# Optimization experiments

Measured on AMD Instinct MI355X. Metric: run time of the kernel, lower is better.

## Reference

```python
import jax, jax.numpy as jnp
import numpy as np

EPS = 1e-5
NEG = -1e20


def layer_norm(x, gamma, beta):
    mu = jnp.mean(x, axis=-1, keepdims=True)
    var = jnp.mean(jnp.square(x - mu), axis=-1, keepdims=True)
    return (x - mu) * jax.lax.rsqrt(var + EPS) * gamma + beta


def setup_inputs() -> dict:
    key = jax.random.key(0)
    ks = jax.random.split(key, 12)
    B, S, D, H, HD = 2, 2048, 1024, 16, 64
    hid = H * HD
    inp = {
        "q": jax.random.normal(ks[0], (B, S, D), jnp.float32),
        "k": jax.random.normal(ks[1], (B, S, D), jnp.float32),
        "v": jax.random.normal(ks[2], (B, S, D), jnp.float32),
        "mask": jax.random.randint(ks[3], (B, 1, S, S), 0, 2, jnp.int32),
        "Wq": jax.random.normal(ks[4], (D, hid), jnp.float32) * (D ** -0.5),
        "bq": jnp.zeros((hid,), jnp.float32),
        "Wk": jax.random.normal(ks[5], (D, hid), jnp.float32) * (D ** -0.5),
        "bk": jnp.zeros((hid,), jnp.float32),
        "Wv": jax.random.normal(ks[6], (D, hid), jnp.float32) * (D ** -0.5),
        "bv": jnp.zeros((hid,), jnp.float32),
        "Wo": jax.random.normal(ks[7], (hid, D), jnp.float32) * (hid ** -0.5),
        "bo": jnp.zeros((D,), jnp.float32),
        "gamma": jnp.ones((D,), jnp.float32),
        "beta": jnp.zeros((D,), jnp.float32),
    }
    return inp


def reference(q, k, v, mask, Wq, bq, Wk, bk, Wv, bv, Wo, bo, gamma, beta):
    B, S, D = q.shape
    H, HD = 16, 64
    scale = HD ** -0.5
    qh = (layer_norm(q, gamma, beta) @ Wq + bq).reshape(B, S, H, HD).transpose(0, 2, 1, 3)
    kh = (layer_norm(k, gamma, beta) @ Wk + bk).reshape(B, S, H, HD).transpose(0, 2, 1, 3)
    vh = (layer_norm(v, gamma, beta) @ Wv + bv).reshape(B, S, H, HD).transpose(0, 2, 1, 3)
    dots = jnp.einsum('bhqd,bhkd->bhqk', qh, kh)  # [B,H,S,S]
    dots = jnp.where(mask == 0, NEG, dots) * scale  # mask BEFORE scale (as in source)
    attn = jax.nn.softmax(dots, axis=-1)
    out = jnp.einsum('bhqk,bhkd->bhqd', attn, vh)  # [B,H,S,HD]
    # Faithful to `out.view(B, S, -1)` on a [B,H,S,HD]-contiguous tensor: raw reshape,
    # no head transpose.
    out = out.reshape(B, S, H * HD)
    return out @ Wo + bo
```

## Files before the change

### kernel.cpp

```cpp
#include <hip/hip_runtime.h>

typedef short short8 __attribute__((ext_vector_type(8)));
typedef float f32x4 __attribute__((ext_vector_type(4)));

#define QSCALE 0.18033688011112042f

__device__ __forceinline__ unsigned short f2bf(float f) {
  unsigned u = __builtin_bit_cast(unsigned, f);
  u += 0x7fffu + ((u >> 16) & 1u);
  return (unsigned short)(u >> 16);
}

__device__ __forceinline__ void gload16(const void* g, void* l) {
  typedef __attribute__((address_space(1))) unsigned int gas;
  typedef __attribute__((address_space(3))) unsigned int las;
  __builtin_amdgcn_global_load_lds((gas*)(unsigned long long)g,
                                   (las*)(unsigned)(unsigned long long)l, 16, 0, 0);
}

#define MFMA16(a, b, c) __builtin_amdgcn_mfma_f32_16x16x32_bf16(a, b, c, 0, 0, 0)

__global__ __launch_bounds__(256) void wtrans_kernel(
    const float* __restrict__ Wq, const float* __restrict__ Wk,
    const float* __restrict__ Wv, const float* __restrict__ Wo,
    unsigned short* __restrict__ Wt) {
  const int wsel = blockIdx.z;
  const float* W = wsel == 0 ? Wq : wsel == 1 ? Wk : wsel == 2 ? Wv : Wo;
  const float wscale = (wsel == 0) ? QSCALE : 1.0f;
  unsigned short* out = Wt + (long)wsel * 1048576;
  __shared__ float lds[64][65];
  const int t = threadIdx.x;
  const int k0 = blockIdx.x * 64, n0 = blockIdx.y * 64;
#pragma unroll
  for (int i = 0; i < 4; ++i) {
    int r = (t >> 4) + i * 16, c4 = (t & 15) * 4;
    float4 vv = *(const float4*)(W + (long)(k0 + r) * 1024 + n0 + c4);
    lds[r][c4] = vv.x; lds[r][c4 + 1] = vv.y; lds[r][c4 + 2] = vv.z; lds[r][c4 + 3] = vv.w;
  }
  __syncthreads();
#pragma unroll
  for (int i = 0; i < 16; ++i) {
    int flat = t + i * 256;
    int n = flat >> 6, kk = flat & 63;
    out[(long)(n0 + n) * 1024 + k0 + kk] = f2bf(lds[kk][n] * wscale);
  }
}

__global__ __launch_bounds__(256) void maskpack_kernel(const int* __restrict__ mask,
                                                       unsigned* __restrict__ bits) {
  const long n = 8388608;
  const long stride = (long)gridDim.x * 256;
  const int lane = threadIdx.x & 63;
  for (long i = (long)blockIdx.x * 256 + threadIdx.x; i < n; i += stride) {
    unsigned long long bal = __ballot(mask[i] != 0);
    if ((lane & 31) == 0) bits[i >> 5] = (unsigned)(bal >> (lane & 32));
  }
}

__global__ __launch_bounds__(256) void ln_kernel(
    const float* __restrict__ q, const float* __restrict__ k, const float* __restrict__ v,
    const float* __restrict__ gamma, const float* __restrict__ beta,
    unsigned short* __restrict__ lnq, unsigned short* __restrict__ lnk,
    unsigned short* __restrict__ lnv) {
  const int row = blockIdx.x, which = blockIdx.y;
  const float* x = (which == 0 ? q : which == 1 ? k : v) + (long)row * 1024;
  unsigned short* y = (which == 0 ? lnq : which == 1 ? lnk : lnv) + (long)row * 1024;
  const int t = threadIdx.x, lane = t & 63, wv = t >> 6;
  float4 xv = ((const float4*)x)[t];
  float s = xv.x + xv.y + xv.z + xv.w;
  float s2 = xv.x * xv.x + xv.y * xv.y + xv.z * xv.z + xv.w * xv.w;
#pragma unroll
  for (int off = 32; off > 0; off >>= 1) {
    s += __shfl_down(s, off);
    s2 += __shfl_down(s2, off);
  }
  __shared__ float red[8];
  if (lane == 0) { red[wv] = s; red[wv + 4] = s2; }
  __syncthreads();
  float tot = red[0] + red[1] + red[2] + red[3];
  float tot2 = red[4] + red[5] + red[6] + red[7];
  float mu = tot * (1.0f / 1024.0f);
  float var = tot2 * (1.0f / 1024.0f) - mu * mu;
  float rs = rsqrtf(var + 1e-5f);
  float4 g = ((const float4*)gamma)[t];
  float4 be = ((const float4*)beta)[t];
  ushort4 o;
  o.x = f2bf((xv.x - mu) * rs * g.x + be.x);
  o.y = f2bf((xv.y - mu) * rs * g.y + be.y);
  o.z = f2bf((xv.z - mu) * rs * g.z + be.z);
  o.w = f2bf((xv.w - mu) * rs * g.w + be.w);
  ((ushort4*)y)[t] = o;
}

template <int BM, int MODE>
__global__ __launch_bounds__(256) void gemm_kernel(
    const unsigned short* __restrict__ A0, const unsigned short* __restrict__ A1,
    const unsigned short* __restrict__ A2, const unsigned short* __restrict__ Wt,
    const float* __restrict__ b0, const float* __restrict__ b1,
    const float* __restrict__ b2, unsigned short* __restrict__ outB,
    unsigned short* __restrict__ outV, float* __restrict__ outF) {
  constexpr int BK = 64;
  constexpr int MI = BM / 32;
  const int z = blockIdx.z;
  const unsigned short* A = z == 0 ? A0 : z == 1 ? A1 : A2;
  const unsigned short* Bt = Wt + (long)z * 1048576;
  const float* bias = z == 0 ? b0 : z == 1 ? b1 : b2;
  unsigned short* outz = outB + (long)z * 4194304;
  const float bscale = (MODE == 0 && z == 0) ? QSCALE : 1.0f;

  __shared__ char lds[BM * 128 + 16384];
  char* As = lds;
  char* Bs = lds + BM * 128;
  const int tid = threadIdx.x, lane = tid & 63, w = tid >> 6;
  const int wr = w >> 1, wc = w & 1;
  const int m0 = blockIdx.x * BM, n0 = blockIdx.y * 128;
  constexpr int K = 1024;
  constexpr int ACH = BM * 8 / 256;

  f32x4 acc[MI][4] = {};
  for (int kt = 0; kt < K / BK; ++kt) {
    __syncthreads();
#pragma unroll
    for (int i = 0; i < ACH; ++i) {
      int c = tid + i * 256;
      int row = c >> 3, pg = (c & 7) ^ (row & 7);
      gload16(A + (long)(m0 + row) * K + kt * BK + pg * 8, As + c * 16);
    }
#pragma unroll
    for (int i = 0; i < 4; ++i) {
      int c = tid + i * 256;
      int row = c >> 3, pg = (c & 7) ^ (row & 7);
      gload16(Bt + (long)(n0 + row) * K + kt * BK + pg * 8, Bs + c * 16);
    }
    asm volatile("s_waitcnt vmcnt(0)" ::: "memory");
    __syncthreads();
#pragma unroll
    for (int ks = 0; ks < 2; ++ks) {
      short8 af[MI], bf[4];
#pragma unroll
      for (int mi = 0; mi < MI; ++mi) {
        int row = wr * (BM / 2) + mi * 16 + (lane & 15);
        int part = (ks * 4 + (lane >> 4)) ^ (row & 7);
        af[mi] = *(const short8*)(As + row * 128 + part * 16);
      }
#pragma unroll
      for (int ni = 0; ni < 4; ++ni) {
        int row = wc * 64 + ni * 16 + (lane & 15);
        int part = (ks * 4 + (lane >> 4)) ^ (row & 7);
        bf[ni] = *(const short8*)(Bs + row * 128 + part * 16);
      }
#pragma unroll
      for (int mi = 0; mi < MI; ++mi)
#pragma unroll
        for (int ni = 0; ni < 4; ++ni)
          acc[mi][ni] = MFMA16(af[mi], bf[ni], acc[mi][ni]);
    }
  }
#pragma unroll
  for (int mi = 0; mi < MI; ++mi) {
    int mbase = m0 + wr * (BM / 2) + mi * 16 + ((lane >> 4) << 2);
#pragma unroll
    for (int ni = 0; ni < 4; ++ni) {
      int j = n0 + wc * 64 + ni * 16 + (lane & 15);
      float bj = bias[j] * bscale;
      float t0 = acc[mi][ni][0] + bj;
      float t1 = acc[mi][ni][1] + bj;
      float t2 = acc[mi][ni][2] + bj;
      float t3 = acc[mi][ni][3] + bj;
      if constexpr (MODE == 0) {
        int b = mbase >> 11, s = mbase & 2047;
        int h = j >> 6, d = j & 63;
        if (z == 2) {
          unsigned lo, hi;
          asm("v_cvt_pk_bf16_f32 %0, %1, %2" : "=v"(lo) : "v"(t0), "v"(t1));
          asm("v_cvt_pk_bf16_f32 %0, %1, %2" : "=v"(hi) : "v"(t2), "v"(t3));
          uint2 o; o.x = lo; o.y = hi;
          *(uint2*)(outV + ((long)(b * 16 + h) * 64 + d) * 2048 + s) = o;
        } else {
          long base = (((long)(b * 16 + h)) * 2048 + s) * 64 + d;
          outz[base] = f2bf(t0);
          outz[base + 64] = f2bf(t1);
          outz[base + 128] = f2bf(t2);
          outz[base + 192] = f2bf(t3);
        }
      } else {
        outF[(long)mbase * 1024 + j] = t0;
        outF[(long)(mbase + 1) * 1024 + j] = t1;
        outF[(long)(mbase + 2) * 1024 + j] = t2;
        outF[(long)(mbase + 3) * 1024 + j] = t3;
      }
    }
  }
}

__global__ __launch_bounds__(256, 4) void attn_kernel(
    const unsigned short* __restrict__ qh, const unsigned short* __restrict__ kh,
    const unsigned short* __restrict__ vt, const unsigned* __restrict__ mbits,
    unsigned short* __restrict__ O) {
  constexpr int S = 2048, NT = 32;
  __shared__ char lds[40960];
  char* Ks = lds;
  char* Vts = lds + 16384;
  const int tid = threadIdx.x, lane = tid & 63, w = tid >> 6;
  const int g = lane >> 4, c = lane & 15;
  char* Pw = lds + 32768 + w * 2048;

  const int flat = blockIdx.y * 32 + blockIdx.x;
  const int fl2 = (flat & 7) * 128 + (flat >> 3);
  const int qb = fl2 & 31, bh = fl2 >> 5, b = bh >> 4;

  const unsigned short* qp = qh + (long)bh * S * 64;
  const unsigned short* kp = kh + (long)bh * S * 64;
  const unsigned short* vp = vt + (long)bh * 64 * S;
  unsigned short* op = O + (long)bh * S * 64;
  const unsigned* mrow = mbits + (long)b * S * 64;
  const int q0 = qb * 64 + w * 16;
  const int myq = q0 + c;

  short8 bq_[2];
#pragma unroll
  for (int ds = 0; ds < 2; ++ds)
    bq_[ds] = *(const short8*)(qp + (long)myq * 64 + ds * 32 + g * 8);

  f32x4 o_acc[4] = {};
  float lpart = 0.f;

#define STAGE(KT, BUF)                                                              \
  {                                                                                 \
    _Pragma("unroll") for (int i = 0; i < 2; ++i) {                                 \
      int cc = tid + i * 256;                                                       \
      int row = cc >> 3, pg = (cc & 7) ^ (row & 7);                                 \
      gload16(kp + (long)((KT)*64 + row) * 64 + pg * 8, Ks + (BUF)*8192 + cc * 16); \
    }                                                                               \
    _Pragma("unroll") for (int i = 0; i < 2; ++i) {                                 \
      int cc = tid + i * 256;                                                       \
      int row = cc >> 3, pg = (cc & 7) ^ (row & 7);                                 \
      gload16(vp + (long)row * S + (KT)*64 + pg * 8, Vts + (BUF)*8192 + cc * 16);   \
    }                                                                               \
  }

  STAGE(0, 0);
  uint2 mcur = *(const uint2*)(mrow + (long)myq * 64);
  uint2 mnxt = mcur;

  for (int kt = 0; kt < NT; ++kt) {
    const int cur = kt & 1;
    if (kt + 1 < NT) {
      STAGE(kt + 1, cur ^ 1);
      mnxt = *(const uint2*)(mrow + (long)myq * 64 + (kt + 1) * 2);
      asm volatile("s_waitcnt vmcnt(5)" ::: "memory");
    } else {
      asm volatile("s_waitcnt vmcnt(0)" ::: "memory");
    }
    __builtin_amdgcn_s_barrier();

    f32x4 sc[4] = {};
    const char* Kb = Ks + cur * 8192;
    __builtin_amdgcn_s_setprio(1);
#pragma unroll
    for (int ds = 0; ds < 2; ++ds) {
#pragma unroll
      for (int kf = 0; kf < 4; ++kf) {
        int row = kf * 16 + c;
        int part = (ds * 4 + g) ^ (row & 7);
        short8 ak = *(const short8*)(Kb + row * 128 + part * 16);
        sc[kf] = MFMA16(ak, bq_[ds], sc[kf]);
      }
    }
    __builtin_amdgcn_s_setprio(0);

    unsigned ws0 = mcur.x >> (g * 4), ws1 = mcur.y >> (g * 4);
#pragma unroll
    for (int kf = 0; kf < 4; ++kf) {
      unsigned wsh = ((kf >= 2) ? ws1 : ws0) >> ((kf & 1) * 16);
      float pv0 = __builtin_amdgcn_exp2f(sc[kf][0]);
      float pv1 = __builtin_amdgcn_exp2f(sc[kf][1]);
      float pv2 = __builtin_amdgcn_exp2f(sc[kf][2]);
      float pv3 = __builtin_amdgcn_exp2f(sc[kf][3]);
      pv0 = (wsh & 1u) ? pv0 : 0.f;
      pv1 = (wsh & 2u) ? pv1 : 0.f;
      pv2 = (wsh & 4u) ? pv2 : 0.f;
      pv3 = (wsh & 8u) ? pv3 : 0.f;
      lpart += (pv0 + pv1) + (pv2 + pv3);
      unsigned plo, phi;
      asm("v_cvt_pk_bf16_f32 %0, %1, %2" : "=v"(plo) : "v"(pv0), "v"(pv1));
      asm("v_cvt_pk_bf16_f32 %0, %1, %2" : "=v"(phi) : "v"(pv2), "v"(pv3));
      uint2 pk2; pk2.x = plo; pk2.y = phi;
      int plog = kf * 2 + (g >> 1);
      *(uint2*)(Pw + c * 128 + ((plog ^ (c & 7)) * 16) + (g & 1) * 8) = pk2;
    }
    mcur = mnxt;

    const char* Vb = Vts + cur * 8192;
    __builtin_amdgcn_s_setprio(1);
#pragma unroll
    for (int ks = 0; ks < 2; ++ks) {
      int part = ks * 4 + g;
      short8 pa = *(const short8*)(Pw + c * 128 + ((part ^ (c & 7)) * 16));
#pragma unroll
      for (int nd = 0; nd < 4; ++nd) {
        int d = nd * 16 + c;
        short8 bv = *(const short8*)(Vb + d * 128 + ((part ^ (d & 7)) * 16));
        o_acc[nd] = MFMA16(pa, bv, o_acc[nd]);
      }
    }
    __builtin_amdgcn_s_setprio(0);

    asm volatile("s_waitcnt lgkmcnt(0)" ::: "memory");
    __builtin_amdgcn_sched_barrier(0);
    __builtin_amdgcn_s_barrier();
  }
#undef STAGE

  lpart += __shfl_xor(lpart, 16);
  lpart += __shfl_xor(lpart, 32);
#pragma unroll
  for (int r = 0; r < 4; ++r) {
    float lr = __shfl(lpart, g * 4 + r);
    float inv = 1.0f / lr;
    int qrow = q0 + g * 4 + r;
#pragma unroll
    for (int nd = 0; nd < 4; ++nd)
      op[(long)qrow * 64 + nd * 16 + c] = f2bf(o_acc[nd][r] * inv);
  }
}

extern "C" void kernel_launch(void* const* d_in, const int* in_sizes, int n_in,
                              void* d_out, int out_size, void* d_ws, size_t ws_size,
                              hipStream_t stream) {
  const float* q = (const float*)d_in[0];
  const float* k = (const float*)d_in[1];
  const float* v = (const float*)d_in[2];
  const int* mask = (const int*)d_in[3];
  const float* Wq = (const float*)d_in[4];
  const float* bq = (const float*)d_in[5];
  const float* Wk = (const float*)d_in[6];
  const float* bk = (const float*)d_in[7];
  const float* Wv = (const float*)d_in[8];
  const float* bv = (const float*)d_in[9];
  const float* Wo = (const float*)d_in[10];
  const float* bo = (const float*)d_in[11];
  const float* gamma = (const float*)d_in[12];
  const float* beta = (const float*)d_in[13];
  float* out = (float*)d_out;

  char* ws = (char*)d_ws;
  unsigned short* Wt = (unsigned short*)ws;
  unsigned* mbits = (unsigned*)(ws + 8u * 1024 * 1024);
  unsigned short* lnq = (unsigned short*)(ws + 9u * 1024 * 1024);
  unsigned short* lnk = lnq + 4194304;
  unsigned short* lnv = lnk + 4194304;
  unsigned short* qh = lnv + 4194304;
  unsigned short* kh = qh + 4194304;
  unsigned short* vtb = kh + 4194304;
  unsigned short* Ob = lnq;

  wtrans_kernel<<<dim3(16, 16, 4), 256, 0, stream>>>(Wq, Wk, Wv, Wo, Wt);
  maskpack_kernel<<<1024, 256, 0, stream>>>(mask, mbits);
  ln_kernel<<<dim3(4096, 3), 256, 0, stream>>>(q, k, v, gamma, beta, lnq, lnk, lnv);
  gemm_kernel<128, 0><<<dim3(32, 8, 3), 256, 0, stream>>>(lnq, lnk, lnv, Wt, bq, bk, bv,
                                                          qh, vtb, nullptr);
  attn_kernel<<<dim3(32, 32), 256, 0, stream>>>(qh, kh, vtb, mbits, Ob);
  gemm_kernel<64, 1><<<dim3(64, 8, 1), 256, 0, stream>>>(Ob, Ob, Ob, Wt + 3 * 1048576,
                                                         bo, bo, bo, nullptr, nullptr, out);
}
```

Baseline: 152.5 us.

## Double query rows per attention warp and unroll kv loop by two

Each attention wave now handles 32 query rows instead of 16, so each K and V fragment loaded from LDS feeds two MFMAs. This halves the number of blocks and the K/V staging traffic per query. The kv loop is manually unrolled over the two LDS buffers. The output GEMM also switches to the 128-row tile configuration. The costs are more registers and LDS per block, lower occupancy (launch bounds drop from 4 to 2 blocks), and fewer blocks to fill the GPU.

```diff
diff --git a/kernel.cpp b/kernel.cpp
--- a/kernel.cpp
+++ b/kernel.cpp
@@ -193,37 +193,39 @@
   }
 }
 
-__global__ __launch_bounds__(256, 4) void attn_kernel(
+__global__ __launch_bounds__(256, 2) void attn_kernel(
     const unsigned short* __restrict__ qh, const unsigned short* __restrict__ kh,
     const unsigned short* __restrict__ vt, const unsigned* __restrict__ mbits,
     unsigned short* __restrict__ O) {
   constexpr int S = 2048, NT = 32;
-  __shared__ char lds[40960];
+  __shared__ char lds[49152];
   char* Ks = lds;
   char* Vts = lds + 16384;
   const int tid = threadIdx.x, lane = tid & 63, w = tid >> 6;
   const int g = lane >> 4, c = lane & 15;
-  char* Pw = lds + 32768 + w * 2048;
-
-  const int flat = blockIdx.y * 32 + blockIdx.x;
-  const int fl2 = (flat & 7) * 128 + (flat >> 3);
-  const int qb = fl2 & 31, bh = fl2 >> 5, b = bh >> 4;
+  char* Pw = lds + 32768 + w * 4096;
+
+  const int flat = blockIdx.y * 16 + blockIdx.x;
+  const int fl2 = (flat & 7) * 64 + (flat >> 3);
+  const int qb = fl2 & 15, bh = fl2 >> 4, b = bh >> 4;
 
   const unsigned short* qp = qh + (long)bh * S * 64;
   const unsigned short* kp = kh + (long)bh * S * 64;
   const unsigned short* vp = vt + (long)bh * 64 * S;
   unsigned short* op = O + (long)bh * S * 64;
   const unsigned* mrow = mbits + (long)b * S * 64;
-  const int q0 = qb * 64 + w * 16;
-  const int myq = q0 + c;
-
-  short8 bq_[2];
-#pragma unroll
-  for (int ds = 0; ds < 2; ++ds)
-    bq_[ds] = *(const short8*)(qp + (long)myq * 64 + ds * 32 + g * 8);
-
-  f32x4 o_acc[4] = {};
-  float lpart = 0.f;
+  const int q0 = qb * 128 + w * 32;
+  const int myq0 = q0 + c, myq1 = q0 + 16 + c;
+
+  short8 bq_[2][2];
+#pragma unroll
+  for (int qg = 0; qg < 2; ++qg)
+#pragma unroll
+    for (int ds = 0; ds < 2; ++ds)
+      bq_[qg][ds] = *(const short8*)(qp + (long)(q0 + qg * 16 + c) * 64 + ds * 32 + g * 8);
+
+  f32x4 o_acc[2][4] = {};
+  float lp0 = 0.f, lp1 = 0.f;
 
 #define STAGE(KT, BUF)                                                              \
   {                                                                                 \
@@ -239,89 +241,109 @@
     }                                                                               \
   }
 
+#define SOFTMAX(SC, MC, LP, QG)                                                     \
+  {                                                                                 \
+    unsigned ws0 = MC.x >> (g * 4), ws1 = MC.y >> (g * 4);                          \
+    _Pragma("unroll") for (int kf = 0; kf < 4; ++kf) {                              \
+      unsigned wsh = ((kf >= 2) ? ws1 : ws0) >> ((kf & 1) * 16);                    \
+      float pv0 = __builtin_amdgcn_exp2f(SC[kf][0]);                                \
+      float pv1 = __builtin_amdgcn_exp2f(SC[kf][1]);                                \
+      float pv2 = __builtin_amdgcn_exp2f(SC[kf][2]);                                \
+      float pv3 = __builtin_amdgcn_exp2f(SC[kf][3]);                                \
+      pv0 = (wsh & 1u) ? pv0 : 0.f;                                                 \
+      pv1 = (wsh & 2u) ? pv1 : 0.f;                                                 \
+      pv2 = (wsh & 4u) ? pv2 : 0.f;                                                 \
+      pv3 = (wsh & 8u) ? pv3 : 0.f;                                                 \
+      LP += (pv0 + pv1) + (pv2 + pv3);                                              \
+      unsigned plo, phi;                                                            \
+      asm("v_cvt_pk_bf16_f32 %0, %1, %2" : "=v"(plo) : "v"(pv0), "v"(pv1));         \
+      asm("v_cvt_pk_bf16_f32 %0, %1, %2" : "=v"(phi) : "v"(pv2), "v"(pv3));         \
+      uint2 pk2; pk2.x = plo; pk2.y = phi;                                          \
+      int plog = kf * 2 + (g >> 1);                                                 \
+      *(uint2*)(Pw + (QG)*2048 + c * 128 + ((plog ^ (c & 7)) * 16) + (g & 1) * 8) = \
+          pk2;                                                                      \
+    }                                                                               \
+  }
+
+#define SUBSTEP(BUF, MC0, MC1)                                                      \
+  {                                                                                 \
+    f32x4 sc0[4] = {}, sc1[4] = {};                                                 \
+    const char* Kb = Ks + (BUF)*8192;                                               \
+    __builtin_amdgcn_s_setprio(1);                                                  \
+    _Pragma("unroll") for (int ds = 0; ds < 2; ++ds) {                              \
+      _Pragma("unroll") for (int kf = 0; kf < 4; ++kf) {                            \
+        int row = kf * 16 + c;                                                      \
+        int part = (ds * 4 + g) ^ (c & 7);                                          \
+        short8 ak = *(const short8*)(Kb + row * 128 + part * 16);                   \
+        sc0[kf] = MFMA16(ak, bq_[0][ds], sc0[kf]);                                  \
+        sc1[kf] = MFMA16(ak, bq_[1][ds], sc1[kf]);                                  \
+      }                                                                             \
+    }                                                                               \
+    __builtin_amdgcn_s_setprio(0);                                                  \
+    SOFTMAX(sc0, MC0, lp0, 0);                                                      \
+    SOFTMAX(sc1, MC1, lp1, 1);                                                      \
+    const char* Vb = Vts + (BUF)*8192;                                              \
+    __builtin_amdgcn_s_setprio(1);                                                  \
+    _Pragma("unroll") for (int ks = 0; ks < 2; ++ks) {                              \
+      int part = ks * 4 + g;                                                        \
+      short8 pa0 = *(const short8*)(Pw + c * 128 + ((part ^ (c & 7)) * 16));        \
+      short8 pa1 = *(const short8*)(Pw + 2048 + c * 128 + ((part ^ (c & 7)) * 16)); \
+      _Pragma("unroll") for (int nd = 0; nd < 4; ++nd) {                            \
+        int d = nd * 16 + c;                                                        \
+        short8 bv = *(const short8*)(Vb + d * 128 + ((part ^ (d & 7)) * 16));       \
+        o_acc[0][nd] = MFMA16(pa0, bv, o_acc[0][nd]);                               \
+        o_acc[1][nd] = MFMA16(pa1, bv, o_acc[1][nd]);                               \
+      }                                                                             \
+    }                                                                               \
+    __builtin_amdgcn_s_setprio(0);                                                  \
+    asm volatile("s_waitcnt lgkmcnt(0)" ::: "memory");                              \
+    __builtin_amdgcn_s_barrier();                                                   \
+  }
+
   STAGE(0, 0);
-  uint2 mcur = *(const uint2*)(mrow + (long)myq * 64);
-  uint2 mnxt = mcur;
-
-  for (int kt = 0; kt < NT; ++kt) {
-    const int cur = kt & 1;
-    if (kt + 1 < NT) {
-      STAGE(kt + 1, cur ^ 1);
-      mnxt = *(const uint2*)(mrow + (long)myq * 64 + (kt + 1) * 2);
-      asm volatile("s_waitcnt vmcnt(5)" ::: "memory");
+  uint2 m0c = *(const uint2*)(mrow + (long)myq0 * 64);
+  uint2 m1c = *(const uint2*)(mrow + (long)myq1 * 64);
+  uint2 m0n, m1n;
+
+  for (int kt2 = 0; kt2 < NT; kt2 += 2) {
+    STAGE(kt2 + 1, 1);
+    m0n = *(const uint2*)(mrow + (long)myq0 * 64 + (kt2 + 1) * 2);
+    m1n = *(const uint2*)(mrow + (long)myq1 * 64 + (kt2 + 1) * 2);
+    asm volatile("s_waitcnt vmcnt(6)" ::: "memory");
+    __builtin_amdgcn_s_barrier();
+    SUBSTEP(0, m0c, m1c);
+    if (kt2 + 2 < NT) {
+      STAGE(kt2 + 2, 0);
+      m0c = *(const uint2*)(mrow + (long)myq0 * 64 + (kt2 + 2) * 2);
+      m1c = *(const uint2*)(mrow + (long)myq1 * 64 + (kt2 + 2) * 2);
+      asm volatile("s_waitcnt vmcnt(6)" ::: "memory");
     } else {
       asm volatile("s_waitcnt vmcnt(0)" ::: "memory");
     }
     __builtin_amdgcn_s_barrier();
-
-    f32x4 sc[4] = {};
-    const char* Kb = Ks + cur * 8192;
-    __builtin_amdgcn_s_setprio(1);
-#pragma unroll
-    for (int ds = 0; ds < 2; ++ds) {
-#pragma unroll
-      for (int kf = 0; kf < 4; ++kf) {
-        int row = kf * 16 + c;
-        int part = (ds * 4 + g) ^ (row & 7);
-        short8 ak = *(const short8*)(Kb + row * 128 + part * 16);
-        sc[kf] = MFMA16(ak, bq_[ds], sc[kf]);
-      }
-    }
-    __builtin_amdgcn_s_setprio(0);
-
-    unsigned ws0 = mcur.x >> (g * 4), ws1 = mcur.y >> (g * 4);
-#pragma unroll
-    for (int kf = 0; kf < 4; ++kf) {
-      unsigned wsh = ((kf >= 2) ? ws1 : ws0) >> ((kf & 1) * 16);
-      float pv0 = __builtin_amdgcn_exp2f(sc[kf][0]);
-      float pv1 = __builtin_amdgcn_exp2f(sc[kf][1]);
-      float pv2 = __builtin_amdgcn_exp2f(sc[kf][2]);
-      float pv3 = __builtin_amdgcn_exp2f(sc[kf][3]);
-      pv0 = (wsh & 1u) ? pv0 : 0.f;
-      pv1 = (wsh & 2u) ? pv1 : 0.f;
-      pv2 = (wsh & 4u) ? pv2 : 0.f;
-      pv3 = (wsh & 8u) ? pv3 : 0.f;
-      lpart += (pv0 + pv1) + (pv2 + pv3);
-      unsigned plo, phi;
-      asm("v_cvt_pk_bf16_f32 %0, %1, %2" : "=v"(plo) : "v"(pv0), "v"(pv1));
-      asm("v_cvt_pk_bf16_f32 %0, %1, %2" : "=v"(phi) : "v"(pv2), "v"(pv3));
-      uint2 pk2; pk2.x = plo; pk2.y = phi;
-      int plog = kf * 2 + (g >> 1);
-      *(uint2*)(Pw + c * 128 + ((plog ^ (c & 7)) * 16) + (g & 1) * 8) = pk2;
-    }
-    mcur = mnxt;
-
-    const char* Vb = Vts + cur * 8192;
-    __builtin_amdgcn_s_setprio(1);
-#pragma unroll
-    for (int ks = 0; ks < 2; ++ks) {
-      int part = ks * 4 + g;
-      short8 pa = *(const short8*)(Pw + c * 128 + ((part ^ (c & 7)) * 16));
-#pragma unroll
-      for (int nd = 0; nd < 4; ++nd) {
-        int d = nd * 16 + c;
-        short8 bv = *(const short8*)(Vb + d * 128 + ((part ^ (d & 7)) * 16));
-        o_acc[nd] = MFMA16(pa, bv, o_acc[nd]);
-      }
-    }
-    __builtin_amdgcn_s_setprio(0);
-
-    asm volatile("s_waitcnt lgkmcnt(0)" ::: "memory");
-    __builtin_amdgcn_sched_barrier(0);
-    __builtin_amdgcn_s_barrier();
-  }
+    SUBSTEP(1, m0n, m1n);
+  }
+#undef SUBSTEP
+#undef SOFTMAX
 #undef STAGE
 
-  lpart += __shfl_xor(lpart, 16);
-  lpart += __shfl_xor(lpart, 32);
+  lp0 += __shfl_xor(lp0, 16);
+  lp0 += __shfl_xor(lp0, 32);
+  lp1 += __shfl_xor(lp1, 16);
+  lp1 += __shfl_xor(lp1, 32);
 #pragma unroll
   for (int r = 0; r < 4; ++r) {
-    float lr = __shfl(lpart, g * 4 + r);
-    float inv = 1.0f / lr;
-    int qrow = q0 + g * 4 + r;
-#pragma unroll
-    for (int nd = 0; nd < 4; ++nd)
-      op[(long)qrow * 64 + nd * 16 + c] = f2bf(o_acc[nd][r] * inv);
+    float lr0 = __shfl(lp0, g * 4 + r);
+    float lr1 = __shfl(lp1, g * 4 + r);
+    float inv0 = 1.0f / lr0;
+    float inv1 = 1.0f / lr1;
+    int qrow0 = q0 + g * 4 + r;
+    int qrow1 = q0 + 16 + g * 4 + r;
+#pragma unroll
+    for (int nd = 0; nd < 4; ++nd) {
+      op[(long)qrow0 * 64 + nd * 16 + c] = f2bf(o_acc[0][nd][r] * inv0);
+      op[(long)qrow1 * 64 + nd * 16 + c] = f2bf(o_acc[1][nd][r] * inv1);
+    }
   }
 }
 
@@ -360,7 +382,7 @@
   ln_kernel<<<dim3(4096, 3), 256, 0, stream>>>(q, k, v, gamma, beta, lnq, lnk, lnv);
   gemm_kernel<128, 0><<<dim3(32, 8, 3), 256, 0, stream>>>(lnq, lnk, lnv, Wt, bq, bk, bv,
                                                           qh, vtb, nullptr);
-  attn_kernel<<<dim3(32, 32), 256, 0, stream>>>(qh, kh, vtb, mbits, Ob);
-  gemm_kernel<64, 1><<<dim3(64, 8, 1), 256, 0, stream>>>(Ob, Ob, Ob, Wt + 3 * 1048576,
-                                                         bo, bo, bo, nullptr, nullptr, out);
-}
+  attn_kernel<<<dim3(16, 32), 256, 0, stream>>>(qh, kh, vtb, mbits, Ob);
+  gemm_kernel<128, 1><<<dim3(32, 8, 1), 256, 0, stream>>>(Ob, Ob, Ob, Wt + 3 * 1048576,
+                                                          bo, bo, bo, nullptr, nullptr, out);
+}
```

New measurement: 157.5 us. 3.3% more time.

## Load K fragments directly to registers in attention, enlarge output GEMM tile

Applied to the files above, without the earlier changes.

The attention kernel stops staging K tiles through LDS and instead loads each wave's K MFMA operands straight from global memory into registers, prefetching the next tile after the QK MFMAs. This shrinks LDS use from 40 KB to 24 KB per block and removes the K LDS writes and reads, at the cost of more VGPRs and redundant global loads of K across the four waves. The vmcnt wait is adjusted to the new count of outstanding loads and a sched_barrier is dropped. Separately, the output projection GEMM switches from a 64-row tile to a 128-row tile with half the blocks.

```diff
diff --git a/kernel.cpp b/kernel.cpp
--- a/kernel.cpp
+++ b/kernel.cpp
@@ -198,12 +198,11 @@
     const unsigned short* __restrict__ vt, const unsigned* __restrict__ mbits,
     unsigned short* __restrict__ O) {
   constexpr int S = 2048, NT = 32;
-  __shared__ char lds[40960];
-  char* Ks = lds;
-  char* Vts = lds + 16384;
+  __shared__ char lds[24576];
+  char* Vts = lds;
   const int tid = threadIdx.x, lane = tid & 63, w = tid >> 6;
   const int g = lane >> 4, c = lane & 15;
-  char* Pw = lds + 32768 + w * 2048;
+  char* Pw = lds + 16384 + w * 2048;
 
   const int flat = blockIdx.y * 32 + blockIdx.x;
   const int fl2 = (flat & 7) * 128 + (flat >> 3);
@@ -225,13 +224,8 @@
   f32x4 o_acc[4] = {};
   float lpart = 0.f;
 
-#define STAGE(KT, BUF)                                                              \
+#define STAGEV(KT, BUF)                                                             \
   {                                                                                 \
-    _Pragma("unroll") for (int i = 0; i < 2; ++i) {                                 \
-      int cc = tid + i * 256;                                                       \
-      int row = cc >> 3, pg = (cc & 7) ^ (row & 7);                                 \
-      gload16(kp + (long)((KT)*64 + row) * 64 + pg * 8, Ks + (BUF)*8192 + cc * 16); \
-    }                                                                               \
     _Pragma("unroll") for (int i = 0; i < 2; ++i) {                                 \
       int cc = tid + i * 256;                                                       \
       int row = cc >> 3, pg = (cc & 7) ^ (row & 7);                                 \
@@ -239,35 +233,41 @@
     }                                                                               \
   }
 
-  STAGE(0, 0);
+#define LOADK(KT)                                                                   \
+  {                                                                                 \
+    _Pragma("unroll") for (int i = 0; i < 8; ++i) {                                 \
+      kA[i] = *(const short8*)(kp + (((long)(KT)*64 + (i & 3) * 16 + c) << 6) +     \
+                               (i >> 2) * 32 + g * 8);                              \
+    }                                                                               \
+  }
+
+  short8 kA[8];
+  STAGEV(0, 0);
   uint2 mcur = *(const uint2*)(mrow + (long)myq * 64);
   uint2 mnxt = mcur;
+  LOADK(0);
 
   for (int kt = 0; kt < NT; ++kt) {
     const int cur = kt & 1;
     if (kt + 1 < NT) {
-      STAGE(kt + 1, cur ^ 1);
+      STAGEV(kt + 1, cur ^ 1);
       mnxt = *(const uint2*)(mrow + (long)myq * 64 + (kt + 1) * 2);
-      asm volatile("s_waitcnt vmcnt(5)" ::: "memory");
+      asm volatile("s_waitcnt vmcnt(3)" ::: "memory");
     } else {
       asm volatile("s_waitcnt vmcnt(0)" ::: "memory");
     }
     __builtin_amdgcn_s_barrier();
 
     f32x4 sc[4] = {};
-    const char* Kb = Ks + cur * 8192;
     __builtin_amdgcn_s_setprio(1);
 #pragma unroll
-    for (int ds = 0; ds < 2; ++ds) {
-#pragma unroll
-      for (int kf = 0; kf < 4; ++kf) {
-        int row = kf * 16 + c;
-        int part = (ds * 4 + g) ^ (row & 7);
-        short8 ak = *(const short8*)(Kb + row * 128 + part * 16);
-        sc[kf] = MFMA16(ak, bq_[ds], sc[kf]);
-      }
-    }
+    for (int ds = 0; ds < 2; ++ds)
+#pragma unroll
+      for (int kf = 0; kf < 4; ++kf)
+        sc[kf] = MFMA16(kA[ds * 4 + kf], bq_[ds], sc[kf]);
     __builtin_amdgcn_s_setprio(0);
+
+    if (kt + 1 < NT) LOADK(kt + 1);
 
     unsigned ws0 = mcur.x >> (g * 4), ws1 = mcur.y >> (g * 4);
 #pragma unroll
@@ -307,10 +307,10 @@
     __builtin_amdgcn_s_setprio(0);
 
     asm volatile("s_waitcnt lgkmcnt(0)" ::: "memory");
-    __builtin_amdgcn_sched_barrier(0);
     __builtin_amdgcn_s_barrier();
   }
-#undef STAGE
+#undef LOADK
+#undef STAGEV
 
   lpart += __shfl_xor(lpart, 16);
   lpart += __shfl_xor(lpart, 32);
@@ -361,6 +361,6 @@
   gemm_kernel<128, 0><<<dim3(32, 8, 3), 256, 0, stream>>>(lnq, lnk, lnv, Wt, bq, bk, bv,
                                                           qh, vtb, nullptr);
   attn_kernel<<<dim3(32, 32), 256, 0, stream>>>(qh, kh, vtb, mbits, Ob);
-  gemm_kernel<64, 1><<<dim3(64, 8, 1), 256, 0, stream>>>(Ob, Ob, Ob, Wt + 3 * 1048576,
-                                                         bo, bo, bo, nullptr, nullptr, out);
-}
+  gemm_kernel<128, 1><<<dim3(32, 8, 1), 256, 0, stream>>>(Ob, Ob, Ob, Wt + 3 * 1048576,
+                                                          bo, bo, bo, nullptr, nullptr, out);
+}
```

New measurement: 244.0 us. 1.6x slower.
